# Performance work log

Measured on AMD Instinct MI355X. Metric: run time of the kernel, lower is better.

## Reference

```python
import jax, jax.numpy as jnp
import numpy as np

B, T, D = 4, 1024, 1024       # batch, tokens, emb_size
E, K, F_EXP = 8, 2, 1024      # num_expert, num_expert_active, expert_size
NUM_BLOCK = 12


def setup_inputs() -> dict:
    key = jax.random.key(0)
    k_x, k_b, k_r, k_1, k_2 = jax.random.split(key, 5)
    x = jax.random.normal(k_x, (B, T, D), dtype=jnp.float32)
    auxfree_bias = jax.random.normal(k_b, (E,), dtype=jnp.float32) * 0.1
    router_w = jax.random.normal(k_r, (E, D), dtype=jnp.float32) * 0.02
    # GroupedLinear weight{i}: [out_features, in_features], applied as x @ W^T
    w1 = jax.random.normal(k_1, (E, F_EXP, D), dtype=jnp.float32) * 0.02
    w2 = jax.random.normal(k_2, (E, D, F_EXP), dtype=jnp.float32) * (0.02 / np.sqrt(2.0 * NUM_BLOCK))
    return {"x": x, "auxfree_bias": auxfree_bias, "router_w": router_w, "w1": w1, "w2": w2}


def reference(x, auxfree_bias, router_w, w1, w2):
    # --- routing: top-k on bias-adjusted DETACHED logits, gather raw logits ---
    logits = jnp.einsum("btd,ed->bte", x, router_w)              # [B,T,E]
    biased = jax.lax.stop_gradient(logits) + auxfree_bias        # bias only affects selection
    _, idx = jax.lax.top_k(biased, K)                            # [B,T,K] int32
    gathered = jnp.take_along_axis(logits, idx, axis=-1)         # [B,T,K]
    probs = jax.nn.softmax(gathered, axis=-1)                    # [B,T,K]

    # combine weights per expert: sum_k probs_k * 1[idx_k == e]  -> [B,T,E]
    combine = jnp.sum(jax.nn.one_hot(idx, E, dtype=x.dtype) * probs[..., None], axis=2)

    # --- experts: out = sum_e combine_e * (gelu(x W1_e^T) W2_e^T) ---
    # (dense per-expert reference for the dispatch -> grouped GEMM -> combine pipeline;
    #  tokens with combine weight 0 contribute nothing, matching the sparse original)
    out = jnp.zeros_like(x)
    for e in range(E):
        h = jax.nn.gelu(jnp.einsum("btd,fd->btf", x, w1[e]), approximate=False)
        out = out + combine[:, :, e:e + 1] * jnp.einsum("btf,df->btd", h, w2[e])
    return out
```

## Files before the change

### kernel.cpp

```cpp
#include <hip/hip_runtime.h>
#include <hip/hip_bf16.h>

#define D_DIM 1024
#define F_DIM 1024
#define NTOK  4096
#define NEXP  8
#define CAP   4096

typedef __attribute__((ext_vector_type(8))) short bf16x8;
typedef __attribute__((ext_vector_type(4))) float f32x4;
typedef __attribute__((ext_vector_type(8))) unsigned short u16x8;

__device__ __forceinline__ unsigned short f2bf(float f) {
    unsigned int u = __float_as_uint(f);
    u = u + 0x7fffu + ((u >> 16) & 1u);
    return (unsigned short)(u >> 16);
}

__device__ __forceinline__ void async_copy16(void* lds, const void* gsrc) {
    __builtin_amdgcn_global_load_lds(
        (const __attribute__((address_space(1))) unsigned int*)gsrc,
        (__attribute__((address_space(3))) unsigned int*)lds, 16, 0, 0);
}

__global__ __launch_bounds__(256) void cvt_kernel(const float* __restrict__ in,
                                                  unsigned short* __restrict__ out, int n) {
    int i = (blockIdx.x * 256 + threadIdx.x) * 8;
    if (i >= n) return;
    const float4* p = (const float4*)(in + i);
    float4 a = p[0], b = p[1];
    u16x8 r;
    r[0] = f2bf(a.x); r[1] = f2bf(a.y); r[2] = f2bf(a.z); r[3] = f2bf(a.w);
    r[4] = f2bf(b.x); r[5] = f2bf(b.y); r[6] = f2bf(b.z); r[7] = f2bf(b.w);
    *(u16x8*)(out + i) = r;
}

__global__ __launch_bounds__(256) void logits_kernel(
    const float* __restrict__ x, const float* __restrict__ rw,
    float* __restrict__ logits)
{
    const int wave = threadIdx.x >> 6, lane = threadIdx.x & 63;
    const int t = blockIdx.x * 4 + wave;
    double s[NEXP];
    #pragma unroll
    for (int e = 0; e < NEXP; ++e) s[e] = 0.0;
    const float* xp = x + (size_t)t * D_DIM;
    for (int kk = 0; kk < D_DIM; kk += 64) {
        float xv = xp[kk + lane];
        #pragma unroll
        for (int e = 0; e < NEXP; ++e)
            s[e] += (double)xv * (double)rw[e * D_DIM + kk + lane];
    }
    #pragma unroll
    for (int e = 0; e < NEXP; ++e) {
        double v = s[e];
        for (int off = 32; off; off >>= 1) v += __shfl_xor(v, off, 64);
        s[e] = v;
    }
    if (lane == 0) {
        #pragma unroll
        for (int e = 0; e < NEXP; ++e) logits[(size_t)t * NEXP + e] = (float)s[e];
    }
}

__global__ __launch_bounds__(256) void assign_kernel(
    const float* __restrict__ logits, const float* __restrict__ bias,
    int* counts, int* list, float* wlist)
{
    __shared__ int lcnt[NEXP];
    __shared__ int lbase[NEXP];
    const int tid = threadIdx.x;
    const int t = blockIdx.x * 256 + tid;
    if (tid < NEXP) lcnt[tid] = 0;
    __syncthreads();

    float lg[NEXP], b2[NEXP];
    #pragma unroll
    for (int e = 0; e < NEXP; ++e) {
        lg[e] = logits[(size_t)t * NEXP + e];
        b2[e] = lg[e] + bias[e];
    }
    int i0 = 0; float b0v = b2[0], l0v = lg[0];
    #pragma unroll
    for (int e = 1; e < NEXP; ++e)
        if (b2[e] > b0v) { b0v = b2[e]; l0v = lg[e]; i0 = e; }
    int i1 = -1; float b1v = 0.f, l1v = 0.f;
    #pragma unroll
    for (int e = 0; e < NEXP; ++e) {
        if (e == i0) continue;
        bool take = (i1 < 0) || (b2[e] > b1v);
        if (take) { i1 = e; b1v = b2[e]; l1v = lg[e]; }
    }
    float m = fmaxf(l0v, l1v);
    float e0 = expf(l0v - m), e1 = expf(l1v - m);
    float inv = 1.0f / (e0 + e1);

    int lp0 = atomicAdd(&lcnt[i0], 1);
    int lp1 = atomicAdd(&lcnt[i1], 1);
    __syncthreads();
    if (tid < NEXP) lbase[tid] = atomicAdd(&counts[tid], lcnt[tid]);
    __syncthreads();

    int p0 = lbase[i0] + lp0;
    list[i0 * CAP + p0] = t; wlist[i0 * CAP + p0] = e0 * inv;
    int p1 = lbase[i1] + lp1;
    list[i1 * CAP + p1] = t; wlist[i1 * CAP + p1] = e1 * inv;
}

__global__ void scan_kernel(const int* __restrict__ counts, int* __restrict__ offs) {
    if (threadIdx.x == 0) {
        int a = 0;
        for (int e = 0; e < NEXP; ++e) { offs[e] = a; a += counts[e]; }
        offs[NEXP] = a;
    }
}

__global__ __launch_bounds__(256) void gemm1_kernel(
    const unsigned short* __restrict__ xb,
    const unsigned short* __restrict__ w1b,
    const int* __restrict__ counts, const int* __restrict__ offs,
    const int* __restrict__ list,
    unsigned short* __restrict__ H)
{
    const int e  = blockIdx.y >> 5;
    const int rb = blockIdx.y & 31;
    const int ne = counts[e];
    if (rb * 128 >= ne) return;
    const int row0 = rb * 128;
    const int n0 = blockIdx.x * 128;
    const int hbase = offs[e];

    __shared__ __align__(16) unsigned short As[128 * 32];
    __shared__ __align__(16) unsigned short Bs[128 * 32];
    __shared__ int toks[128];

    const int tid = threadIdx.x;
    if (tid < 128) {
        int i = row0 + tid;
        if (i >= ne) i = ne - 1;
        toks[tid] = list[e * CAP + i];
    }
    __syncthreads();

    const int wave = tid >> 6, lane = tid & 63;
    const int wr = wave >> 1, wc = wave & 1;

    const int c0 = wave, c1 = wave + 4;
    const int lrow = lane >> 2;
    const int lcol = (lane & 3) * 8;
    const int ar0 = c0 * 16 + lrow;
    const int ar1 = c1 * 16 + lrow;
    const unsigned short* a0 = xb + (size_t)toks[ar0] * D_DIM + lcol;
    const unsigned short* a1 = xb + (size_t)toks[ar1] * D_DIM + lcol;
    const unsigned short* bp = w1b + (size_t)e * F_DIM * D_DIM;
    const unsigned short* b0 = bp + (size_t)(n0 + ar0) * D_DIM + lcol;
    const unsigned short* b1 = bp + (size_t)(n0 + ar1) * D_DIM + lcol;

    unsigned short* Ad0 = &As[c0 * 512];
    unsigned short* Ad1 = &As[c1 * 512];
    unsigned short* Bd0 = &Bs[c0 * 512];
    unsigned short* Bd1 = &Bs[c1 * 512];

    f32x4 acc[4][4];
    #pragma unroll
    for (int m = 0; m < 4; ++m)
        #pragma unroll
        for (int n = 0; n < 4; ++n) acc[m][n] = (f32x4){0.f, 0.f, 0.f, 0.f};

    const int arow = lane & 15;
    const int kg = (lane >> 4) * 8;

    for (int k0 = 0; k0 < D_DIM; k0 += 32) {
        async_copy16(Ad0, a0 + k0);
        async_copy16(Ad1, a1 + k0);
        async_copy16(Bd0, b0 + k0);
        async_copy16(Bd1, b1 + k0);
        __syncthreads();
        bf16x8 af[4], bfr[4];
        #pragma unroll
        for (int m = 0; m < 4; ++m)
            af[m] = *(const bf16x8*)&As[(wr * 64 + m * 16 + arow) * 32 + kg];
        #pragma unroll
        for (int n = 0; n < 4; ++n)
            bfr[n] = *(const bf16x8*)&Bs[(wc * 64 + n * 16 + arow) * 32 + kg];
        #pragma unroll
        for (int m = 0; m < 4; ++m)
            #pragma unroll
            for (int n = 0; n < 4; ++n)
                acc[m][n] = __builtin_amdgcn_mfma_f32_16x16x32_bf16(af[m], bfr[n], acc[m][n], 0, 0, 0);
        __syncthreads();
    }

    #pragma unroll
    for (int m = 0; m < 4; ++m) {
        #pragma unroll
        for (int j = 0; j < 4; ++j) {
            int ri = wr * 64 + m * 16 + (lane >> 4) * 4 + j;
            int i = row0 + ri;
            if (i < ne) {
                unsigned short* hp = H + (size_t)(hbase + i) * F_DIM + n0 + wc * 64;
                #pragma unroll
                for (int n = 0; n < 4; ++n) {
                    float v = acc[m][n][j];
                    float g = 0.5f * v * (1.0f + erff(v * 0.70710678118654752f));
                    hp[n * 16 + (lane & 15)] = f2bf(g);
                }
            }
        }
    }
}

__global__ __launch_bounds__(256) void gemm2_kernel(
    const unsigned short* __restrict__ H,
    const unsigned short* __restrict__ w2b,
    const int* __restrict__ counts, const int* __restrict__ offs,
    const int* __restrict__ list, const float* __restrict__ wlist,
    float* __restrict__ out)
{
    const int e  = blockIdx.y >> 5;
    const int rb = blockIdx.y & 31;
    const int ne = counts[e];
    if (rb * 128 >= ne) return;
    const int row0 = rb * 128;
    const int n0 = blockIdx.x * 128;
    const int hbase = offs[e];

    __shared__ __align__(16) unsigned short As[128 * 32];
    __shared__ __align__(16) unsigned short Bs[128 * 32];
    __shared__ int toks[128];
    __shared__ float wts[128];

    const int tid = threadIdx.x;
    if (tid < 128) {
        int i = row0 + tid;
        if (i >= ne) i = ne - 1;
        toks[tid] = list[e * CAP + i];
        wts[tid]  = wlist[e * CAP + i];
    }
    __syncthreads();

    const int wave = tid >> 6, lane = tid & 63;
    const int wr = wave >> 1, wc = wave & 1;

    const int c0 = wave, c1 = wave + 4;
    const int lrow = lane >> 2;
    const int lcol = (lane & 3) * 8;
    const int ar0 = c0 * 16 + lrow;
    const int ar1 = c1 * 16 + lrow;
    const unsigned short* a0 = H + (size_t)(hbase + row0 + ar0) * F_DIM + lcol;
    const unsigned short* a1 = H + (size_t)(hbase + row0 + ar1) * F_DIM + lcol;
    const unsigned short* bp = w2b + (size_t)e * D_DIM * F_DIM;
    const unsigned short* b0 = bp + (size_t)(n0 + ar0) * F_DIM + lcol;
    const unsigned short* b1 = bp + (size_t)(n0 + ar1) * F_DIM + lcol;

    unsigned short* Ad0 = &As[c0 * 512];
    unsigned short* Ad1 = &As[c1 * 512];
    unsigned short* Bd0 = &Bs[c0 * 512];
    unsigned short* Bd1 = &Bs[c1 * 512];

    f32x4 acc[4][4];
    #pragma unroll
    for (int m = 0; m < 4; ++m)
        #pragma unroll
        for (int n = 0; n < 4; ++n) acc[m][n] = (f32x4){0.f, 0.f, 0.f, 0.f};

    const int arow = lane & 15;
    const int kg = (lane >> 4) * 8;

    for (int k0 = 0; k0 < F_DIM; k0 += 32) {
        async_copy16(Ad0, a0 + k0);
        async_copy16(Ad1, a1 + k0);
        async_copy16(Bd0, b0 + k0);
        async_copy16(Bd1, b1 + k0);
        __syncthreads();
        bf16x8 af[4], bfr[4];
        #pragma unroll
        for (int m = 0; m < 4; ++m)
            af[m] = *(const bf16x8*)&As[(wr * 64 + m * 16 + arow) * 32 + kg];
        #pragma unroll
        for (int n = 0; n < 4; ++n)
            bfr[n] = *(const bf16x8*)&Bs[(wc * 64 + n * 16 + arow) * 32 + kg];
        #pragma unroll
        for (int m = 0; m < 4; ++m)
            #pragma unroll
            for (int n = 0; n < 4; ++n)
                acc[m][n] = __builtin_amdgcn_mfma_f32_16x16x32_bf16(af[m], bfr[n], acc[m][n], 0, 0, 0);
        __syncthreads();
    }

    #pragma unroll
    for (int m = 0; m < 4; ++m) {
        #pragma unroll
        for (int j = 0; j < 4; ++j) {
            int ri = wr * 64 + m * 16 + (lane >> 4) * 4 + j;
            int i = row0 + ri;
            if (i < ne) {
                int t = toks[ri];
                float wt = wts[ri];
                float* op = out + (size_t)t * D_DIM + n0 + wc * 64;
                #pragma unroll
                for (int n = 0; n < 4; ++n)
                    atomicAdd(&op[n * 16 + (lane & 15)], wt * acc[m][n][j]);
            }
        }
    }
}

extern "C" void kernel_launch(void* const* d_in, const int* in_sizes, int n_in,
                              void* d_out, int out_size, void* d_ws, size_t ws_size,
                              hipStream_t stream)
{
    const float* x    = (const float*)d_in[0];
    const float* bias = (const float*)d_in[1];
    const float* rw   = (const float*)d_in[2];
    const float* w1   = (const float*)d_in[3];
    const float* w2   = (const float*)d_in[4];
    float* out = (float*)d_out;

    char* ws = (char*)d_ws;
    size_t cur = 0;
    auto alloc = [&](size_t bytes) -> void* {
        void* p = (void*)(ws + cur);
        cur += (bytes + 255) & ~(size_t)255;
        return p;
    };
    unsigned short* xb   = (unsigned short*)alloc((size_t)NTOK * D_DIM * 2);
    unsigned short* w1b  = (unsigned short*)alloc((size_t)NEXP * F_DIM * D_DIM * 2);
    unsigned short* w2b  = (unsigned short*)alloc((size_t)NEXP * F_DIM * D_DIM * 2);
    unsigned short* Hb   = (unsigned short*)alloc((size_t)(NTOK * 2 + 128) * F_DIM * 2);
    float* logits = (float*)alloc((size_t)NTOK * NEXP * 4);
    int*   list   = (int*)alloc(NEXP * CAP * 4);
    float* wlist  = (float*)alloc(NEXP * CAP * 4);
    int*   counts = (int*)alloc(64);
    int*   offs   = (int*)alloc(64);

    hipMemsetAsync(counts, 0, 64, stream);
    hipMemsetAsync(out, 0, (size_t)out_size * 4, stream);

    cvt_kernel<<<NTOK * D_DIM / 2048, 256, 0, stream>>>(x, xb, NTOK * D_DIM);
    cvt_kernel<<<NEXP * F_DIM * D_DIM / 2048, 256, 0, stream>>>(w1, w1b, NEXP * F_DIM * D_DIM);
    cvt_kernel<<<NEXP * F_DIM * D_DIM / 2048, 256, 0, stream>>>(w2, w2b, NEXP * F_DIM * D_DIM);
    logits_kernel<<<NTOK / 4, 256, 0, stream>>>(x, rw, logits);
    assign_kernel<<<NTOK / 256, 256, 0, stream>>>(logits, bias, counts, list, wlist);
    scan_kernel<<<1, 64, 0, stream>>>(counts, offs);
    gemm1_kernel<<<dim3(8, 256), 256, 0, stream>>>(xb, w1b, counts, offs, list, Hb);
    gemm2_kernel<<<dim3(8, 256), 256, 0, stream>>>(Hb, w2b, counts, offs, list, wlist, out);
}
```

Before: 235.2 us.

## Double-buffer LDS tiles with BK=64 and XOR swizzle in both expert GEMMs

Both grouped GEMM kernels now use two LDS buffers with a K-step of 64. The next tile is issued via async global-to-LDS copies while the current one is computed, which halves the number of barriers and overlaps global latency with MFMA work. An XOR swizzle on the 16-byte column chunks is applied on store and read, to avoid LDS bank conflicts on the wider 64-element rows. LDS use grows to 64 KB per block, which may reduce occupancy.

```diff
diff --git a/kernel.cpp b/kernel.cpp
--- a/kernel.cpp
+++ b/kernel.cpp
@@ -115,6 +115,36 @@
     }
 }
 
+#define STAGE(AB, BB, k0)                                                   \
+    do {                                                                    \
+        _Pragma("unroll")                                                   \
+        for (int i = 0; i < 4; ++i) {                                       \
+            async_copy16(&AB[(wave * 4 + i) * 512], ap[i] + (k0));          \
+            async_copy16(&BB[(wave * 4 + i) * 512], bp_[i] + (k0));         \
+        }                                                                   \
+    } while (0)
+
+#define COMPUTE(AB, BB)                                                     \
+    do {                                                                    \
+        _Pragma("unroll")                                                   \
+        for (int kk = 0; kk < 2; ++kk) {                                    \
+            bf16x8 af[4], bfv[4];                                           \
+            const int sbase = kk * 4 + (lane >> 4);                         \
+            const int phys  = (sbase ^ (lane & 7)) * 8;                     \
+            _Pragma("unroll")                                               \
+            for (int m = 0; m < 4; ++m)                                     \
+                af[m] = *(const bf16x8*)&AB[(wr * 64 + m * 16 + (lane & 15)) * 64 + phys]; \
+            _Pragma("unroll")                                               \
+            for (int n = 0; n < 4; ++n)                                     \
+                bfv[n] = *(const bf16x8*)&BB[(wc * 64 + n * 16 + (lane & 15)) * 64 + phys]; \
+            _Pragma("unroll")                                               \
+            for (int m = 0; m < 4; ++m)                                     \
+                _Pragma("unroll")                                           \
+                for (int n = 0; n < 4; ++n)                                 \
+                    acc[m][n] = __builtin_amdgcn_mfma_f32_16x16x32_bf16(af[m], bfv[n], acc[m][n], 0, 0, 0); \
+        }                                                                   \
+    } while (0)
+
 __global__ __launch_bounds__(256) void gemm1_kernel(
     const unsigned short* __restrict__ xb,
     const unsigned short* __restrict__ w1b,
@@ -130,8 +160,8 @@
     const int n0 = blockIdx.x * 128;
     const int hbase = offs[e];
 
-    __shared__ __align__(16) unsigned short As[128 * 32];
-    __shared__ __align__(16) unsigned short Bs[128 * 32];
+    __shared__ __align__(16) unsigned short As0[128 * 64], As1[128 * 64];
+    __shared__ __align__(16) unsigned short Bs0[128 * 64], Bs1[128 * 64];
     __shared__ int toks[128];
 
     const int tid = threadIdx.x;
@@ -145,21 +175,17 @@
     const int wave = tid >> 6, lane = tid & 63;
     const int wr = wave >> 1, wc = wave & 1;
 
-    const int c0 = wave, c1 = wave + 4;
-    const int lrow = lane >> 2;
-    const int lcol = (lane & 3) * 8;
-    const int ar0 = c0 * 16 + lrow;
-    const int ar1 = c1 * 16 + lrow;
-    const unsigned short* a0 = xb + (size_t)toks[ar0] * D_DIM + lcol;
-    const unsigned short* a1 = xb + (size_t)toks[ar1] * D_DIM + lcol;
-    const unsigned short* bp = w1b + (size_t)e * F_DIM * D_DIM;
-    const unsigned short* b0 = bp + (size_t)(n0 + ar0) * D_DIM + lcol;
-    const unsigned short* b1 = bp + (size_t)(n0 + ar1) * D_DIM + lcol;
-
-    unsigned short* Ad0 = &As[c0 * 512];
-    unsigned short* Ad1 = &As[c1 * 512];
-    unsigned short* Bd0 = &Bs[c0 * 512];
-    unsigned short* Bd1 = &Bs[c1 * 512];
+    const int lr  = lane >> 3;
+    const int swz = ((lane & 7) ^ lr) * 8;
+    const unsigned short* ap[4];
+    const unsigned short* bp_[4];
+    const unsigned short* wbase = w1b + (size_t)e * F_DIM * D_DIM;
+    #pragma unroll
+    for (int i = 0; i < 4; ++i) {
+        int r = wave * 32 + i * 8 + lr;
+        ap[i]  = xb + (size_t)toks[r] * D_DIM + swz;
+        bp_[i] = wbase + (size_t)(n0 + r) * D_DIM + swz;
+    }
 
     f32x4 acc[4][4];
     #pragma unroll
@@ -167,29 +193,20 @@
         #pragma unroll
         for (int n = 0; n < 4; ++n) acc[m][n] = (f32x4){0.f, 0.f, 0.f, 0.f};
 
-    const int arow = lane & 15;
-    const int kg = (lane >> 4) * 8;
-
-    for (int k0 = 0; k0 < D_DIM; k0 += 32) {
-        async_copy16(Ad0, a0 + k0);
-        async_copy16(Ad1, a1 + k0);
-        async_copy16(Bd0, b0 + k0);
-        async_copy16(Bd1, b1 + k0);
+    STAGE(As0, Bs0, 0);
+    __syncthreads();
+    for (int t = 0; t < 7; ++t) {
+        STAGE(As1, Bs1, t * 128 + 64);
+        COMPUTE(As0, Bs0);
         __syncthreads();
-        bf16x8 af[4], bfr[4];
-        #pragma unroll
-        for (int m = 0; m < 4; ++m)
-            af[m] = *(const bf16x8*)&As[(wr * 64 + m * 16 + arow) * 32 + kg];
-        #pragma unroll
-        for (int n = 0; n < 4; ++n)
-            bfr[n] = *(const bf16x8*)&Bs[(wc * 64 + n * 16 + arow) * 32 + kg];
-        #pragma unroll
-        for (int m = 0; m < 4; ++m)
-            #pragma unroll
-            for (int n = 0; n < 4; ++n)
-                acc[m][n] = __builtin_amdgcn_mfma_f32_16x16x32_bf16(af[m], bfr[n], acc[m][n], 0, 0, 0);
+        STAGE(As0, Bs0, t * 128 + 128);
+        COMPUTE(As1, Bs1);
         __syncthreads();
     }
+    STAGE(As1, Bs1, 960);
+    COMPUTE(As0, Bs0);
+    __syncthreads();
+    COMPUTE(As1, Bs1);
 
     #pragma unroll
     for (int m = 0; m < 4; ++m) {
@@ -225,8 +242,8 @@
     const int n0 = blockIdx.x * 128;
     const int hbase = offs[e];
 
-    __shared__ __align__(16) unsigned short As[128 * 32];
-    __shared__ __align__(16) unsigned short Bs[128 * 32];
+    __shared__ __align__(16) unsigned short As0[128 * 64], As1[128 * 64];
+    __shared__ __align__(16) unsigned short Bs0[128 * 64], Bs1[128 * 64];
     __shared__ int toks[128];
     __shared__ float wts[128];
 
@@ -242,21 +259,17 @@
     const int wave = tid >> 6, lane = tid & 63;
     const int wr = wave >> 1, wc = wave & 1;
 
-    const int c0 = wave, c1 = wave + 4;
-    const int lrow = lane >> 2;
-    const int lcol = (lane & 3) * 8;
-    const int ar0 = c0 * 16 + lrow;
-    const int ar1 = c1 * 16 + lrow;
-    const unsigned short* a0 = H + (size_t)(hbase + row0 + ar0) * F_DIM + lcol;
-    const unsigned short* a1 = H + (size_t)(hbase + row0 + ar1) * F_DIM + lcol;
-    const unsigned short* bp = w2b + (size_t)e * D_DIM * F_DIM;
-    const unsigned short* b0 = bp + (size_t)(n0 + ar0) * F_DIM + lcol;
-    const unsigned short* b1 = bp + (size_t)(n0 + ar1) * F_DIM + lcol;
-
-    unsigned short* Ad0 = &As[c0 * 512];
-    unsigned short* Ad1 = &As[c1 * 512];
-    unsigned short* Bd0 = &Bs[c0 * 512];
-    unsigned short* Bd1 = &Bs[c1 * 512];
+    const int lr  = lane >> 3;
+    const int swz = ((lane & 7) ^ lr) * 8;
+    const unsigned short* ap[4];
+    const unsigned short* bp_[4];
+    const unsigned short* wbase = w2b + (size_t)e * D_DIM * F_DIM;
+    #pragma unroll
+    for (int i = 0; i < 4; ++i) {
+        int r = wave * 32 + i * 8 + lr;
+        ap[i]  = H + (size_t)(hbase + row0 + r) * F_DIM + swz;
+        bp_[i] = wbase + (size_t)(n0 + r) * F_DIM + swz;
+    }
 
     f32x4 acc[4][4];
     #pragma unroll
@@ -264,29 +277,20 @@
         #pragma unroll
         for (int n = 0; n < 4; ++n) acc[m][n] = (f32x4){0.f, 0.f, 0.f, 0.f};
 
-    const int arow = lane & 15;
-    const int kg = (lane >> 4) * 8;
-
-    for (int k0 = 0; k0 < F_DIM; k0 += 32) {
-        async_copy16(Ad0, a0 + k0);
-        async_copy16(Ad1, a1 + k0);
-        async_copy16(Bd0, b0 + k0);
-        async_copy16(Bd1, b1 + k0);
+    STAGE(As0, Bs0, 0);
+    __syncthreads();
+    for (int t = 0; t < 7; ++t) {
+        STAGE(As1, Bs1, t * 128 + 64);
+        COMPUTE(As0, Bs0);
         __syncthreads();
-        bf16x8 af[4], bfr[4];
-        #pragma unroll
-        for (int m = 0; m < 4; ++m)
-            af[m] = *(const bf16x8*)&As[(wr * 64 + m * 16 + arow) * 32 + kg];
-        #pragma unroll
-        for (int n = 0; n < 4; ++n)
-            bfr[n] = *(const bf16x8*)&Bs[(wc * 64 + n * 16 + arow) * 32 + kg];
-        #pragma unroll
-        for (int m = 0; m < 4; ++m)
-            #pragma unroll
-            for (int n = 0; n < 4; ++n)
-                acc[m][n] = __builtin_amdgcn_mfma_f32_16x16x32_bf16(af[m], bfr[n], acc[m][n], 0, 0, 0);
+        STAGE(As0, Bs0, t * 128 + 128);
+        COMPUTE(As1, Bs1);
         __syncthreads();
     }
+    STAGE(As1, Bs1, 960);
+    COMPUTE(As0, Bs0);
+    __syncthreads();
+    COMPUTE(As1, Bs1);
 
     #pragma unroll
     for (int m = 0; m < 4; ++m) {
```

Result: slower. 251.3 us (+6.8%).
